# Kernel optimization log

Hardware: AMD Instinct MI355X
Metric: run time of the kernel (lower is better)

## Reference

```python
import jax, jax.numpy as jnp
import numpy as np

H = 768
NH = 12
HD = H // NH  # 64


def setup_inputs() -> dict:
    key = jax.random.key(0)
    ks = jax.random.split(key, 8)
    B, S = 4, 2048
    sc = 1.0 / np.sqrt(H)
    return {
        "hidden_states": jax.random.normal(ks[0], (B, S, H), dtype=jnp.float32),
        "attention_mask": jnp.zeros((B, 1, 1, S), dtype=jnp.float32),
        "Wq": jax.random.normal(ks[1], (H, H), dtype=jnp.float32) * sc,
        "bq": jnp.zeros((H,), dtype=jnp.float32),
        "Wk": jax.random.normal(ks[2], (H, H), dtype=jnp.float32) * sc,
        "bk": jnp.zeros((H,), dtype=jnp.float32),
        "Wv": jax.random.normal(ks[3], (H, H), dtype=jnp.float32) * sc,
        "bv": jnp.zeros((H,), dtype=jnp.float32),
    }


def _split_heads(x):
    # [B,S,H] -> [B,NH,S,HD]
    B, S, _ = x.shape
    return x.reshape(B, S, NH, HD).transpose(0, 2, 1, 3)


def reference(hidden_states, attention_mask, Wq, bq, Wk, bk, Wv, bv):
    q = _split_heads(hidden_states @ Wq + bq)
    k = _split_heads(hidden_states @ Wk + bk)
    v = _split_heads(hidden_states @ Wv + bv)
    # scores: [B,NH,S,S]
    scores = jnp.einsum("bhqd,bhkd->bhqk", q, k) / np.sqrt(HD)
    scores = scores + attention_mask
    probs = jax.nn.softmax(scores, axis=-1)  # dropout is identity in eval
    ctx = jnp.einsum("bhqk,bhkd->bhqd", probs, v)
    B, _, S, _ = ctx.shape
    return ctx.transpose(0, 2, 1, 3).reshape(B, S, H)
```

## Files before the change

kernel.cpp:

```cpp
#include <hip/hip_runtime.h>
#include <stdint.h>

typedef short bf16x8 __attribute__((ext_vector_type(8)));
typedef float f32x4  __attribute__((ext_vector_type(4)));
typedef unsigned short u16;

#define B_  4
#define S_  2048
#define H_  768
#define NH_ 12
#define HD_ 64
#define NPROJ_N (3*H_)
#define PSW 72

static __device__ __forceinline__ u16 f2bf(float f) {
    union { float f; unsigned int u; } x; x.f = f;
    return (u16)((x.u + 0x8000u) >> 16);
}
static __device__ __forceinline__ bf16x8 ld8(const u16* p) {
    return *(const bf16x8*)(const void*)p;
}
static __device__ __forceinline__ void st8(u16* p, bf16x8 v) {
    *(bf16x8*)(void*)p = v;
}
static __device__ __forceinline__ void async_ld16(const u16* g, const short* l) {
    __builtin_amdgcn_global_load_lds(
        (__attribute__((address_space(1))) void*)g,
        (__attribute__((address_space(3))) void*)l,
        16, 0, 0);
}

__global__ __launch_bounds__(256) void prep_kernel(const float* __restrict__ in,
                                                   u16* __restrict__ out,
                                                   const float* __restrict__ wq,
                                                   const float* __restrict__ wk,
                                                   const float* __restrict__ wv,
                                                   u16* __restrict__ wt) {
    __shared__ float t[32][33];
    const int blk = blockIdx.x;
    const int tid = threadIdx.x;
    if (blk < 6144) {
        int i = (blk * 256 + tid) * 4;
        float4 v = *(const float4*)(in + i);
        ushort4 o;
        o.x = f2bf(v.x); o.y = f2bf(v.y); o.z = f2bf(v.z); o.w = f2bf(v.w);
        *(ushort4*)(out + i) = o;
    } else {
        const int idx  = blk - 6144;
        const int proj = idx / 576;
        const int rem  = idx % 576;
        const int bx = rem % 24, by = rem / 24;
        const float* w = (proj == 0) ? wq : (proj == 1) ? wk : wv;
        u16* o = wt + (size_t)proj * H_ * H_;
        const int tx = tid & 31, ty = tid >> 5;
        const int n0 = bx * 32, k0 = by * 32;
        #pragma unroll
        for (int i = 0; i < 4; i++)
            t[ty + i * 8][tx] = w[(size_t)(k0 + ty + i * 8) * H_ + n0 + tx];
        __syncthreads();
        #pragma unroll
        for (int i = 0; i < 4; i++)
            o[(size_t)(n0 + ty + i * 8) * H_ + k0 + tx] = f2bf(t[tx][ty + i * 8]);
    }
}

__global__ __launch_bounds__(256) void qkv_gemm(const u16* __restrict__ A,
                                                const u16* __restrict__ Wt,
                                                const float* __restrict__ bq,
                                                const float* __restrict__ bk,
                                                const float* __restrict__ bv,
                                                u16* __restrict__ qo,
                                                u16* __restrict__ ko,
                                                u16* __restrict__ vto) {
    __shared__ alignas(16) short SMEM[4][128 * 64];

    const int tid  = threadIdx.x;
    const int wave = tid >> 6;
    const int lane = tid & 63;
    const int quad = lane >> 4;
    const int l16  = lane & 15;
    const int wm   = wave & 1;
    const int wn   = wave >> 1;

    const int id  = blockIdx.x;
    const int xcd = id & 7;
    const int j   = id >> 3;
    const int mi  = j & 7;
    const int ni  = j >> 3;
    const int m0 = (xcd * 8 + mi) * 128;
    const int n0 = ni * 128;

    int stR[4], stC[4];
    #pragma unroll
    for (int jj = 0; jj < 4; jj++) {
        const int lc = wave * 256 + jj * 64 + lane;
        stR[jj] = lc >> 3;
        stC[jj] = ((lc & 7) ^ (stR[jj] & 7)) * 8;
    }
    const int fx0 = (quad ^ (l16 & 7)) * 8;
    const int fx1 = fx0 ^ 32;

    f32x4 acc[4][4];
    #pragma unroll
    for (int i = 0; i < 4; i++)
        #pragma unroll
        for (int jj = 0; jj < 4; jj++) acc[i][jj] = (f32x4)0.0f;

#define GSTAGE(kt_, buf_)                                                                     \
    do {                                                                                      \
        const int kk_ = (kt_) * 64;                                                           \
        _Pragma("unroll")                                                                     \
        for (int jj = 0; jj < 4; jj++) {                                                      \
            async_ld16(A  + (size_t)(m0 + stR[jj]) * H_ + kk_ + stC[jj],                      \
                       &SMEM[(buf_) * 2][(wave * 256 + jj * 64) * 8]);                        \
            async_ld16(Wt + (size_t)(n0 + stR[jj]) * H_ + kk_ + stC[jj],                      \
                       &SMEM[(buf_) * 2 + 1][(wave * 256 + jj * 64) * 8]);                    \
        }                                                                                     \
    } while (0)

    GSTAGE(0, 0);
    __syncthreads();

    for (int kt = 0; kt < 12; kt++) {
        const int cur = kt & 1;
        if (kt + 1 < 12) GSTAGE(kt + 1, cur ^ 1);
        const short* As = SMEM[cur * 2];
        const short* Bs = SMEM[cur * 2 + 1];
        #pragma unroll
        for (int ks = 0; ks < 2; ks++) {
            const int fx = ks ? fx1 : fx0;
            bf16x8 af[4], bfr[4];
            #pragma unroll
            for (int i = 0; i < 4; i++)
                af[i] = *(const bf16x8*)(const void*)&As[(wm * 64 + i * 16 + l16) * 64 + fx];
            #pragma unroll
            for (int jj = 0; jj < 4; jj++)
                bfr[jj] = *(const bf16x8*)(const void*)&Bs[(wn * 64 + jj * 16 + l16) * 64 + fx];
            #pragma unroll
            for (int i = 0; i < 4; i++)
                #pragma unroll
                for (int jj = 0; jj < 4; jj++)
                    acc[i][jj] = __builtin_amdgcn_mfma_f32_16x16x32_bf16(af[i], bfr[jj], acc[i][jj], 0, 0, 0);
        }
        __syncthreads();
    }
#undef GSTAGE

    const int proj  = n0 / H_;
    const int hbase = (n0 % H_) >> 6;
    const float* bias = (proj == 0) ? bq : (proj == 1) ? bk : bv;
    u16* Ct = (u16*)SMEM;

    #pragma unroll
    for (int nj = 0; nj < 4; nj++) {
        const int nl = wn * 64 + nj * 16 + l16;
        const float bv_ = bias[(n0 % H_) + nl];
        #pragma unroll
        for (int mi2 = 0; mi2 < 4; mi2++) {
            #pragma unroll
            for (int r = 0; r < 4; r++) {
                const int ml = wm * 64 + mi2 * 16 + quad * 4 + r;
                const u16 val = f2bf(acc[mi2][nj][r] + bv_);
                if (proj < 2)
                    Ct[ml * 128 + ((nl + (ml & 15) * 8) & 127)] = val;
                else
                    Ct[nl * 128 + ((ml + (nl & 15) * 8) & 127)] = val;
            }
        }
    }
    __syncthreads();

    if (proj < 2) {
        u16* dst0 = (proj == 0) ? qo : ko;
        const int c = tid & 7;
        #pragma unroll
        for (int jj = 0; jj < 8; jj++) {
            const int idx = jj * 32 + (tid >> 3);
            const int ml = idx >> 1, h2 = idx & 1;
            const int nbase = h2 * 64 + c * 8;
            bf16x8 v8 = *(const bf16x8*)(const void*)&Ct[ml * 128 + ((nbase + (ml & 15) * 8) & 127)];
            const int m = m0 + ml;
            const int b = m >> 11, s = m & 2047;
            st8(dst0 + ((size_t)(b * NH_ + hbase + h2) * S_ + s) * HD_ + c * 8, v8);
        }
    } else {
        const int b = m0 >> 11;
        #pragma unroll
        for (int jj = 0; jj < 8; jj++) {
            const int nl = (tid >> 3) + (jj & 3) * 32;
            const int c  = (tid & 7) + (jj >> 2) * 8;
            bf16x8 v8 = *(const bf16x8*)(const void*)&Ct[nl * 128 + ((c * 8 + (nl & 15) * 8) & 127)];
            const int h2 = nl >> 6, d = nl & 63;
            st8(vto + ((size_t)(b * NH_ + hbase + h2) * HD_ + d) * S_ + (m0 & 2047) + c * 8, v8);
        }
    }
}

__global__ __launch_bounds__(512) void attn_kernel(const u16* __restrict__ q,
                                                   const u16* __restrict__ k,
                                                   const u16* __restrict__ vt,
                                                   const float* __restrict__ mask,
                                                   float* __restrict__ out) {
    __shared__ alignas(16) short Ks[2][64 * 64];
    __shared__ alignas(16) short Vs[2][64 * 64];
    __shared__ alignas(16) short Ps[128 * PSW];

    const int tid  = threadIdx.x;
    const int wave = tid >> 6;
    const int lane = tid & 63;
    const int quad = lane >> 4;
    const int l16  = lane & 15;

    const int bh = blockIdx.x;
    const int b  = bh / NH_;
    const int q0 = blockIdx.y * 128;
    const float C1 = 0.125f * 1.44269504f;

    const u16* qbase = q + ((size_t)bh * S_ + q0 + wave * 16 + l16) * HD_;
    bf16x8 qf0 = ld8(qbase + quad * 8);
    bf16x8 qf1 = ld8(qbase + 32 + quad * 8);

    const u16* kbase = k  + (size_t)bh * S_ * HD_;
    const u16* vbase = vt + (size_t)bh * HD_ * S_;

    const int sRow = tid >> 3;
    const int sCol = ((tid & 7) ^ (sRow & 7)) * 8;
    const int kOff = sRow * 64 + sCol;
    const int fx0 = (quad ^ (l16 & 7)) * 8;
    const int fx1 = fx0 ^ 32;

    float lsum[4] = {0.f, 0.f, 0.f, 0.f};
    f32x4 o_acc[4];
    #pragma unroll
    for (int c = 0; c < 4; c++) o_acc[c] = (f32x4)0.0f;

#define STAGE(kt_, buf_)                                                              \
    do {                                                                              \
        async_ld16(kbase + (size_t)(kt_) * 4096 + kOff,        &Ks[buf_][wave * 512]); \
        async_ld16(vbase + (size_t)sRow * S_ + (kt_) * 64 + sCol, &Vs[buf_][wave * 512]); \
    } while (0)

    STAGE(0, 0);
    __syncthreads();

    for (int kt = 0; kt < S_ / 64; kt++) {
        const int cur = kt & 1;
        if (kt + 1 < S_ / 64) STAGE(kt + 1, cur ^ 1);
        const int kk = kt * 64;
        const short* Kc = Ks[cur];
        const short* Vc = Vs[cur];

        f32x4 sacc[4];
        #pragma unroll
        for (int c = 0; c < 4; c++) sacc[c] = (f32x4)0.0f;
        #pragma unroll
        for (int c = 0; c < 4; c++) {
            bf16x8 kf0 = *(const bf16x8*)(const void*)&Kc[(c * 16 + l16) * 64 + fx0];
            sacc[c] = __builtin_amdgcn_mfma_f32_16x16x32_bf16(qf0, kf0, sacc[c], 0, 0, 0);
            bf16x8 kf1 = *(const bf16x8*)(const void*)&Kc[(c * 16 + l16) * 64 + fx1];
            sacc[c] = __builtin_amdgcn_mfma_f32_16x16x32_bf16(qf1, kf1, sacc[c], 0, 0, 0);
        }

        float pv[4][4];
        #pragma unroll
        for (int c = 0; c < 4; c++) {
            const float ml = mask[(size_t)b * S_ + kk + c * 16 + l16] * 1.44269504f;
            #pragma unroll
            for (int r = 0; r < 4; r++) {
                const float p = __builtin_amdgcn_exp2f(sacc[c][r] * C1 + ml);
                pv[c][r] = p;
                lsum[r] += p;
            }
        }

        u16* Pw = (u16*)Ps;
        #pragma unroll
        for (int c = 0; c < 4; c++)
            #pragma unroll
            for (int r = 0; r < 4; r++)
                Pw[(wave * 16 + quad * 4 + r) * PSW + c * 16 + l16] = f2bf(pv[c][r]);

        bf16x8 pa0 = *(const bf16x8*)(const void*)&Ps[(wave * 16 + l16) * PSW + quad * 8];
        bf16x8 pa1 = *(const bf16x8*)(const void*)&Ps[(wave * 16 + l16) * PSW + 32 + quad * 8];
        #pragma unroll
        for (int c2 = 0; c2 < 4; c2++) {
            bf16x8 vb0 = *(const bf16x8*)(const void*)&Vc[(c2 * 16 + l16) * 64 + fx0];
            o_acc[c2] = __builtin_amdgcn_mfma_f32_16x16x32_bf16(pa0, vb0, o_acc[c2], 0, 0, 0);
            bf16x8 vb1 = *(const bf16x8*)(const void*)&Vc[(c2 * 16 + l16) * 64 + fx1];
            o_acc[c2] = __builtin_amdgcn_mfma_f32_16x16x32_bf16(pa1, vb1, o_acc[c2], 0, 0, 0);
        }
        __syncthreads();
    }
#undef STAGE

    const int h = bh % NH_;
    #pragma unroll
    for (int r = 0; r < 4; r++) {
        float l = lsum[r];
        #pragma unroll
        for (int off = 1; off < 16; off <<= 1) l += __shfl_xor(l, off);
        const float linv = 1.0f / l;
        const int s = q0 + wave * 16 + quad * 4 + r;
        #pragma unroll
        for (int c2 = 0; c2 < 4; c2++) {
            const int d = c2 * 16 + l16;
            out[((size_t)b * S_ + s) * H_ + h * 64 + d] = o_acc[c2][r] * linv;
        }
    }
}

extern "C" void kernel_launch(void* const* d_in, const int* in_sizes, int n_in,
                              void* d_out, int out_size, void* d_ws, size_t ws_size,
                              hipStream_t stream) {
    const float* hidden = (const float*)d_in[0];
    const float* amask  = (const float*)d_in[1];
    const float* Wq     = (const float*)d_in[2];
    const float* bq     = (const float*)d_in[3];
    const float* Wk     = (const float*)d_in[4];
    const float* bk     = (const float*)d_in[5];
    const float* Wv     = (const float*)d_in[6];
    const float* bv     = (const float*)d_in[7];
    float* out = (float*)d_out;

    char* ws = (char*)d_ws;
    const size_t sz_hidden = (size_t)B_ * S_ * H_ * 2;
    const size_t sz_wt     = (size_t)NPROJ_N * H_ * 2;
    const size_t sz_qkv    = (size_t)B_ * S_ * H_ * 2;

    u16* hid_bf = (u16*)(ws);
    u16* wt     = (u16*)(ws + sz_hidden);
    u16* qbuf   = (u16*)(ws + sz_hidden + sz_wt);
    u16* kbuf   = (u16*)(ws + sz_hidden + sz_wt + sz_qkv);
    u16* vtbuf  = (u16*)(ws + sz_hidden + sz_wt + 2 * sz_qkv);

    prep_kernel<<<dim3(6144 + 1728), dim3(256), 0, stream>>>(
        hidden, hid_bf, Wq, Wk, Wv, wt);
    qkv_gemm<<<dim3(1152), dim3(256), 0, stream>>>(
        hid_bf, wt, bq, bk, bv, qbuf, kbuf, vtbuf);
    attn_kernel<<<dim3(B_ * NH_, S_ / 128), dim3(512), 0, stream>>>(
        qbuf, kbuf, vtbuf, amask, out);
}
```

Baseline: 219.4 us.

## Process two query sub-tiles per wave in attention, halving block threads

The attention kernel now runs 256 threads per block, and each wave handles 32 query rows (two 16-row sub-tiles) instead of 16. Each K and V fragment read from shared memory therefore feeds two MFMAs, and each thread issues twice as many async loads to stage the tiles. This cuts LDS read traffic per FLOP and the number of waves contending for it, at the cost of more accumulator registers per thread. A launch-bounds occupancy hint of 3 blocks is added.

Result: faster. 213.9 us (-2.5%).

```diff
diff --git a/kernel.cpp b/kernel.cpp
--- a/kernel.cpp
+++ b/kernel.cpp
@@ -196,11 +196,11 @@
     }
 }
 
-__global__ __launch_bounds__(512) void attn_kernel(const u16* __restrict__ q,
-                                                   const u16* __restrict__ k,
-                                                   const u16* __restrict__ vt,
-                                                   const float* __restrict__ mask,
-                                                   float* __restrict__ out) {
+__global__ __launch_bounds__(256, 3) void attn_kernel(const u16* __restrict__ q,
+                                                      const u16* __restrict__ k,
+                                                      const u16* __restrict__ vt,
+                                                      const float* __restrict__ mask,
+                                                      float* __restrict__ out) {
     __shared__ alignas(16) short Ks[2][64 * 64];
     __shared__ alignas(16) short Vs[2][64 * 64];
     __shared__ alignas(16) short Ps[128 * PSW];
@@ -216,28 +216,36 @@
     const int q0 = blockIdx.y * 128;
     const float C1 = 0.125f * 1.44269504f;
 
-    const u16* qbase = q + ((size_t)bh * S_ + q0 + wave * 16 + l16) * HD_;
-    bf16x8 qf0 = ld8(qbase + quad * 8);
-    bf16x8 qf1 = ld8(qbase + 32 + quad * 8);
+    bf16x8 qf[2][2];
+    #pragma unroll
+    for (int qb = 0; qb < 2; qb++) {
+        const u16* qbase = q + ((size_t)bh * S_ + q0 + wave * 32 + qb * 16 + l16) * HD_;
+        qf[qb][0] = ld8(qbase + quad * 8);
+        qf[qb][1] = ld8(qbase + 32 + quad * 8);
+    }
 
     const u16* kbase = k  + (size_t)bh * S_ * HD_;
     const u16* vbase = vt + (size_t)bh * HD_ * S_;
 
     const int sRow = tid >> 3;
     const int sCol = ((tid & 7) ^ (sRow & 7)) * 8;
-    const int kOff = sRow * 64 + sCol;
     const int fx0 = (quad ^ (l16 & 7)) * 8;
     const int fx1 = fx0 ^ 32;
 
-    float lsum[4] = {0.f, 0.f, 0.f, 0.f};
-    f32x4 o_acc[4];
-    #pragma unroll
-    for (int c = 0; c < 4; c++) o_acc[c] = (f32x4)0.0f;
-
-#define STAGE(kt_, buf_)                                                              \
-    do {                                                                              \
-        async_ld16(kbase + (size_t)(kt_) * 4096 + kOff,        &Ks[buf_][wave * 512]); \
-        async_ld16(vbase + (size_t)sRow * S_ + (kt_) * 64 + sCol, &Vs[buf_][wave * 512]); \
+    float lsum[2][4];
+    f32x4 o_acc[2][4];
+    #pragma unroll
+    for (int qb = 0; qb < 2; qb++) {
+        #pragma unroll
+        for (int c = 0; c < 4; c++) { o_acc[qb][c] = (f32x4)0.0f; lsum[qb][c] = 0.f; }
+    }
+
+#define STAGE(kt_, buf_)                                                                         \
+    do {                                                                                         \
+        async_ld16(kbase + (size_t)(kt_) * 4096 + sRow * 64 + sCol,        &Ks[buf_][tid * 8]);  \
+        async_ld16(kbase + (size_t)(kt_) * 4096 + (sRow + 32) * 64 + sCol, &Ks[buf_][2048 + tid * 8]); \
+        async_ld16(vbase + (size_t)sRow * S_ + (kt_) * 64 + sCol,          &Vs[buf_][tid * 8]);  \
+        async_ld16(vbase + (size_t)(sRow + 32) * S_ + (kt_) * 64 + sCol,   &Vs[buf_][2048 + tid * 8]); \
     } while (0)
 
     STAGE(0, 0);
@@ -250,44 +258,54 @@
         const short* Kc = Ks[cur];
         const short* Vc = Vs[cur];
 
-        f32x4 sacc[4];
-        #pragma unroll
-        for (int c = 0; c < 4; c++) sacc[c] = (f32x4)0.0f;
+        f32x4 sacc[2][4];
+        #pragma unroll
+        for (int qb = 0; qb < 2; qb++)
+            #pragma unroll
+            for (int c = 0; c < 4; c++) sacc[qb][c] = (f32x4)0.0f;
         #pragma unroll
         for (int c = 0; c < 4; c++) {
             bf16x8 kf0 = *(const bf16x8*)(const void*)&Kc[(c * 16 + l16) * 64 + fx0];
-            sacc[c] = __builtin_amdgcn_mfma_f32_16x16x32_bf16(qf0, kf0, sacc[c], 0, 0, 0);
+            sacc[0][c] = __builtin_amdgcn_mfma_f32_16x16x32_bf16(qf[0][0], kf0, sacc[0][c], 0, 0, 0);
+            sacc[1][c] = __builtin_amdgcn_mfma_f32_16x16x32_bf16(qf[1][0], kf0, sacc[1][c], 0, 0, 0);
             bf16x8 kf1 = *(const bf16x8*)(const void*)&Kc[(c * 16 + l16) * 64 + fx1];
-            sacc[c] = __builtin_amdgcn_mfma_f32_16x16x32_bf16(qf1, kf1, sacc[c], 0, 0, 0);
-        }
-
-        float pv[4][4];
-        #pragma unroll
-        for (int c = 0; c < 4; c++) {
-            const float ml = mask[(size_t)b * S_ + kk + c * 16 + l16] * 1.44269504f;
-            #pragma unroll
-            for (int r = 0; r < 4; r++) {
-                const float p = __builtin_amdgcn_exp2f(sacc[c][r] * C1 + ml);
-                pv[c][r] = p;
-                lsum[r] += p;
+            sacc[0][c] = __builtin_amdgcn_mfma_f32_16x16x32_bf16(qf[0][1], kf1, sacc[0][c], 0, 0, 0);
+            sacc[1][c] = __builtin_amdgcn_mfma_f32_16x16x32_bf16(qf[1][1], kf1, sacc[1][c], 0, 0, 0);
+        }
+
+        float ml[4];
+        #pragma unroll
+        for (int c = 0; c < 4; c++)
+            ml[c] = mask[(size_t)b * S_ + kk + c * 16 + l16] * 1.44269504f;
+
+        u16* Pw = (u16*)Ps;
+        #pragma unroll
+        for (int qb = 0; qb < 2; qb++) {
+            #pragma unroll
+            for (int c = 0; c < 4; c++) {
+                #pragma unroll
+                for (int r = 0; r < 4; r++) {
+                    const float p = __builtin_amdgcn_exp2f(sacc[qb][c][r] * C1 + ml[c]);
+                    lsum[qb][r] += p;
+                    Pw[(wave * 32 + qb * 16 + quad * 4 + r) * PSW + c * 16 + l16] = f2bf(p);
+                }
             }
         }
 
-        u16* Pw = (u16*)Ps;
-        #pragma unroll
-        for (int c = 0; c < 4; c++)
-            #pragma unroll
-            for (int r = 0; r < 4; r++)
-                Pw[(wave * 16 + quad * 4 + r) * PSW + c * 16 + l16] = f2bf(pv[c][r]);
-
-        bf16x8 pa0 = *(const bf16x8*)(const void*)&Ps[(wave * 16 + l16) * PSW + quad * 8];
-        bf16x8 pa1 = *(const bf16x8*)(const void*)&Ps[(wave * 16 + l16) * PSW + 32 + quad * 8];
+        bf16x8 pa[2][2];
+        #pragma unroll
+        for (int qb = 0; qb < 2; qb++) {
+            pa[qb][0] = *(const bf16x8*)(const void*)&Ps[(wave * 32 + qb * 16 + l16) * PSW + quad * 8];
+            pa[qb][1] = *(const bf16x8*)(const void*)&Ps[(wave * 32 + qb * 16 + l16) * PSW + 32 + quad * 8];
+        }
         #pragma unroll
         for (int c2 = 0; c2 < 4; c2++) {
             bf16x8 vb0 = *(const bf16x8*)(const void*)&Vc[(c2 * 16 + l16) * 64 + fx0];
-            o_acc[c2] = __builtin_amdgcn_mfma_f32_16x16x32_bf16(pa0, vb0, o_acc[c2], 0, 0, 0);
+            o_acc[0][c2] = __builtin_amdgcn_mfma_f32_16x16x32_bf16(pa[0][0], vb0, o_acc[0][c2], 0, 0, 0);
+            o_acc[1][c2] = __builtin_amdgcn_mfma_f32_16x16x32_bf16(pa[1][0], vb0, o_acc[1][c2], 0, 0, 0);
             bf16x8 vb1 = *(const bf16x8*)(const void*)&Vc[(c2 * 16 + l16) * 64 + fx1];
-            o_acc[c2] = __builtin_amdgcn_mfma_f32_16x16x32_bf16(pa1, vb1, o_acc[c2], 0, 0, 0);
+            o_acc[0][c2] = __builtin_amdgcn_mfma_f32_16x16x32_bf16(pa[0][1], vb1, o_acc[0][c2], 0, 0, 0);
+            o_acc[1][c2] = __builtin_amdgcn_mfma_f32_16x16x32_bf16(pa[1][1], vb1, o_acc[1][c2], 0, 0, 0);
         }
         __syncthreads();
     }
@@ -295,16 +313,19 @@
 
     const int h = bh % NH_;
     #pragma unroll
-    for (int r = 0; r < 4; r++) {
-        float l = lsum[r];
-        #pragma unroll
-        for (int off = 1; off < 16; off <<= 1) l += __shfl_xor(l, off);
-        const float linv = 1.0f / l;
-        const int s = q0 + wave * 16 + quad * 4 + r;
-        #pragma unroll
-        for (int c2 = 0; c2 < 4; c2++) {
-            const int d = c2 * 16 + l16;
-            out[((size_t)b * S_ + s) * H_ + h * 64 + d] = o_acc[c2][r] * linv;
+    for (int qb = 0; qb < 2; qb++) {
+        #pragma unroll
+        for (int r = 0; r < 4; r++) {
+            float l = lsum[qb][r];
+            #pragma unroll
+            for (int off = 1; off < 16; off <<= 1) l += __shfl_xor(l, off);
+            const float linv = 1.0f / l;
+            const int s = q0 + wave * 32 + qb * 16 + quad * 4 + r;
+            #pragma unroll
+            for (int c2 = 0; c2 < 4; c2++) {
+                const int d = c2 * 16 + l16;
+                out[((size_t)b * S_ + s) * H_ + h * 64 + d] = o_acc[qb][c2][r] * linv;
+            }
         }
     }
 }
@@ -337,6 +358,6 @@
         hidden, hid_bf, Wq, Wk, Wv, wt);
     qkv_gemm<<<dim3(1152), dim3(256), 0, stream>>>(
         hid_bf, wt, bq, bk, bv, qbuf, kbuf, vtbuf);
-    attn_kernel<<<dim3(B_ * NH_, S_ / 128), dim3(512), 0, stream>>>(
+    attn_kernel<<<dim3(B_ * NH_, S_ / 128), dim3(256), 0, stream>>>(
         qbuf, kbuf, vtbuf, amask, out);
 }
```
